# Kernel tuning notes

Hardware: AMD Instinct MI355X
Metric: run time of the kernel (lower is better)

Reference implementation:

```python
import jax, jax.numpy as jnp
import numpy as np

SCALE_CLS = 7.0
EPS = 1e-12

def _l2norm(x):
    # torch F.normalize: x / max(||x||_2, eps) along last dim
    n = jnp.sqrt(jnp.sum(x * x, axis=-1, keepdims=True))
    return x / jnp.maximum(n, EPS)

def setup_inputs() -> dict:
    key = jax.random.key(0)
    k1, k2 = jax.random.split(key)
    B, Q, C, D, H, W = 4, 75, 5, 512, 6, 6
    ftrain = jax.random.normal(k1, (B, Q, C, D, H, W), dtype=jnp.float32)
    ftest = jax.random.normal(k2, (B, Q, C, D, H, W), dtype=jnp.float32)
    return {"ftrain": ftrain, "ftest": ftest, "K": 28}

def reference(ftrain, ftest, K):
    B, Q, C, D, H, W = ftrain.shape
    P = H * W  # 36 spatial positions
    # spatial means -> [B,Q,C,1,D]
    ftest_mean = ftest.mean(axis=(4, 5))[:, :, :, None, :]
    ftrain_mean = ftrain.mean(axis=(4, 5))[:, :, :, None, :]
    # flatten spatial, move channel last -> [B,Q,C,P,D]
    ft = jnp.swapaxes(ftest.reshape(B, Q, C, D, P), 3, 4)
    fr = jnp.swapaxes(ftrain.reshape(B, Q, C, D, P), 3, 4)
    ft = _l2norm(ft)
    fr = _l2norm(fr)
    ftest_mean = _l2norm(ftest_mean)
    ftrain_mean = _l2norm(ftrain_mean)
    # global scores [B,Q,C]
    scores = SCALE_CLS * jnp.sum(jnp.squeeze(ftest_mean * ftrain_mean), axis=-1)
    # per-position scores [B,Q,C,P]
    ftrain_scores = SCALE_CLS * jnp.sum(ftest_mean * fr, axis=-1)
    ftest_scores = SCALE_CLS * jnp.sum(ft * ftrain_mean, axis=-1)
    # top-K positions (indices distinct, so one-hot-sum mask == gather)
    _, train_ind = jax.lax.top_k(ftrain_scores, K)  # [B,Q,C,K]
    _, test_ind = jax.lax.top_k(ftest_scores, K)
    # gather top-K spatial features and average -> [B,Q,C,D]
    ftest_fuse = jnp.take_along_axis(ft, test_ind[..., None], axis=3).sum(axis=3) / K
    ftrain_fuse = jnp.take_along_axis(fr, train_ind[..., None], axis=3).sum(axis=3) / K
    ftest_fuse = _l2norm(ftest_fuse)
    ftrain_fuse = _l2norm(ftrain_fuse)
    scores_final = SCALE_CLS * jnp.sum(ftest_fuse * ftrain_fuse, axis=-1)
    return (scores, scores_final)
```

## Files before the change

kernel.cpp:

```cpp
#include <hip/hip_runtime.h>
#include <stdint.h>

#define NGRP 1500
#define DD   512
#define PP   36
#define DP   (DD*PP)
#define NT   512
#define SCALE_CLS 7.0f
#define EPS 1e-12f

__device__ __forceinline__ float waveRed(float x){
  #pragma unroll
  for (int off = 32; off; off >>= 1) x += __shfl_xor(x, off, 64);
  return x;
}

__global__ __launch_bounds__(NT, 4)
void topk_fuse(const float* __restrict__ gtrain,
               const float* __restrict__ gtest,
               const int* __restrict__ Kp,
               float* __restrict__ out)
{
  __shared__ float sR[DP];
  __shared__ float s_tm[DD];
  __shared__ float s_q4[4][PP];
  __shared__ float s_a4[4][PP];
  __shared__ float s_e[PP], s_b[PP];
  __shared__ float s_nt[PP], s_nr[PP];
  __shared__ float s_st[PP], s_sr[PP];
  __shared__ __align__(16) float s_wt[PP];
  __shared__ __align__(16) float s_wr[PP];
  __shared__ float s_red[24];

  const int t    = threadIdx.x;
  const int lane = t & 63;
  const int wave = t >> 6;
  const int g    = blockIdx.x;
  const int K    = Kp[0];

  float4 rowT[9];
  {
    const float4* gTrow = (const float4*)(gtest + (size_t)g * DP + (size_t)t * PP);
    #pragma unroll
    for (int i = 0; i < 9; ++i) rowT[i] = gTrow[i];
  }
  {
    const float4* gR4 = (const float4*)(gtrain + (size_t)g * DP);
    float4 r0=gR4[t],        r1=gR4[t+NT],   r2=gR4[t+2*NT], r3=gR4[t+3*NT],
           r4=gR4[t+4*NT],   r5=gR4[t+5*NT], r6=gR4[t+6*NT], r7=gR4[t+7*NT],
           r8=gR4[t+8*NT];
    float4* sR4 = (float4*)sR;
    sR4[t]      = r0; sR4[t+NT]   = r1; sR4[t+2*NT] = r2; sR4[t+3*NT] = r3;
    sR4[t+4*NT] = r4; sR4[t+5*NT] = r5; sR4[t+6*NT] = r6; sR4[t+7*NT] = r7;
    sR4[t+8*NT] = r8;
  }

  if (t < PP) {
    s_e[t] = 0.f; s_b[t] = 0.f;
    #pragma unroll
    for (int v = 0; v < 4; ++v) { s_q4[v][t] = 0.f; s_a4[v][t] = 0.f; }
  }

  float acc = 0.f;
  #pragma unroll
  for (int i = 0; i < 9; ++i) { float4 x = rowT[i]; acc += (x.x + x.y) + (x.z + x.w); }
  const float tm = acc * (1.0f / 36.0f);
  s_tm[t] = tm;

  __syncthreads();

  const float4* rr4 = (const float4*)(sR + t * PP);
  float accr = 0.f;
  #pragma unroll
  for (int i = 0; i < 9; ++i) { float4 y = rr4[i]; accr += (y.x + y.y) + (y.z + y.w); }
  const float rm = accr * (1.0f / 36.0f);

  {
    float pm2 = waveRed(tm * tm);
    float pr2 = waveRed(rm * rm);
    float pmr = waveRed(tm * rm);
    if (lane == 0) { s_red[wave] = pm2; s_red[8+wave] = pr2; s_red[16+wave] = pmr; }
  }

  {
    const int slot = (lane >> 2) & 3;
    #pragma unroll
    for (int i = 0; i < 9; ++i) {
      float4 x = rowT[i];
      #pragma unroll
      for (int cpt = 0; cpt < 4; ++cpt) {
        const float xv = (cpt == 0) ? x.x : (cpt == 1) ? x.y : (cpt == 2) ? x.z : x.w;
        const int p = 4 * i + cpt;
        float q = xv * xv;
        float a = xv * rm;
        q += __shfl_xor(q, 1, 64); q += __shfl_xor(q, 2, 64);
        a += __shfl_xor(a, 1, 64); a += __shfl_xor(a, 2, 64);
        if ((lane & 3) == 0) {
          atomicAdd(&s_q4[slot][p], q);
          atomicAdd(&s_a4[slot][p], a);
        }
      }
    }
  }

  if (t < 504) {
    const int p = t % 36, c = t / 36;
    float e = 0.f, bb = 0.f;
    for (int d = c; d < DD; d += 14) {
      float y = sR[d * PP + p];
      e  += y * y;
      bb += y * s_tm[d];
    }
    atomicAdd(&s_e[p], e); atomicAdd(&s_b[p], bb);
  }
  __syncthreads();

  if (t == 0) {
    float m2 = 0.f, r2 = 0.f, mr = 0.f;
    #pragma unroll
    for (int w = 0; w < 8; ++w) { m2 += s_red[w]; r2 += s_red[8+w]; mr += s_red[16+w]; }
    out[g] = SCALE_CLS * mr / (fmaxf(sqrtf(m2), EPS) * fmaxf(sqrtf(r2), EPS));
  }

  if (wave < 2 && lane < PP) {
    float q, dm;
    if (wave) { q = s_e[lane]; dm = s_b[lane]; }
    else {
      q  = s_q4[0][lane] + s_q4[1][lane] + s_q4[2][lane] + s_q4[3][lane];
      dm = s_a4[0][lane] + s_a4[1][lane] + s_a4[2][lane] + s_a4[3][lane];
    }
    float n  = fmaxf(sqrtf(q), EPS);
    float sc = dm / n;
    if (wave) { s_nr[lane] = n; s_sr[lane] = sc; }
    else      { s_nt[lane] = n; s_st[lane] = sc; }
  }
  __syncthreads();

  if (wave < 2 && lane < PP) {
    const float* sc = wave ? s_sr : s_st;
    const float* nn = wave ? s_nr : s_nt;
    float*       w  = wave ? s_wr : s_wt;
    float mine = sc[lane];
    int rank = 0;
    #pragma unroll
    for (int p = 0; p < PP; ++p) {
      float o = sc[p];
      rank += ((o > mine) || (o == mine && p < lane)) ? 1 : 0;
    }
    w[lane] = (rank < K) ? (1.0f / nn[lane]) : 0.f;
  }
  __syncthreads();

  {
    const float4* w4t = (const float4*)s_wt;
    const float4* w4r = (const float4*)s_wr;
    float U = 0.f, V = 0.f;
    #pragma unroll
    for (int i = 0; i < 9; ++i) {
      float4 x = rowT[i], wa = w4t[i];
      float4 y = rr4[i],  wb = w4r[i];
      U += x.x*wa.x + x.y*wa.y + x.z*wa.z + x.w*wa.w;
      V += y.x*wb.x + y.y*wb.y + y.z*wb.z + y.w*wb.w;
    }
    float u2 = waveRed(U * U);
    float v2 = waveRed(V * V);
    float uv = waveRed(U * V);
    if (lane == 0) { s_red[wave] = u2; s_red[8+wave] = v2; s_red[16+wave] = uv; }
  }
  __syncthreads();
  if (t == 0) {
    float u2 = 0.f, v2 = 0.f, uv = 0.f;
    #pragma unroll
    for (int w = 0; w < 8; ++w) { u2 += s_red[w]; v2 += s_red[8+w]; uv += s_red[16+w]; }
    out[NGRP + g] = SCALE_CLS * uv / (fmaxf(sqrtf(u2), EPS) * fmaxf(sqrtf(v2), EPS));
  }
}

extern "C" void kernel_launch(void* const* d_in, const int* in_sizes, int n_in,
                              void* d_out, int out_size, void* d_ws, size_t ws_size,
                              hipStream_t stream)
{
  const float* ftrain = (const float*)d_in[0];
  const float* ftest  = (const float*)d_in[1];
  const int*   Kp     = (const int*)d_in[2];
  float*       out    = (float*)d_out;
  topk_fuse<<<NGRP, NT, 0, stream>>>(ftrain, ftest, Kp, out);
}
```

Before: 299.4 us.

## Compute all scores from a 72x72 Gram matrix of stacked test/train features

Result: faster. 258.3 us (-13.7%).

```diff
diff --git a/kernel.cpp b/kernel.cpp
--- a/kernel.cpp
+++ b/kernel.cpp
@@ -4,8 +4,13 @@
 #define NGRP 1500
 #define DD   512
 #define PP   36
+#define MW   72
 #define DP   (DD*PP)
-#define NT   512
+#define KC   64
+#define NCH  (DD/KC)
+#define NT   192
+#define NTILE 171
+#define F4C  (KC*PP/4)
 #define SCALE_CLS 7.0f
 #define EPS 1e-12f
 
@@ -21,16 +26,15 @@
                const int* __restrict__ Kp,
                float* __restrict__ out)
 {
-  __shared__ float sR[DP];
-  __shared__ float s_tm[DD];
-  __shared__ float s_q4[4][PP];
-  __shared__ float s_a4[4][PP];
-  __shared__ float s_e[PP], s_b[PP];
+  __shared__ __align__(16) float sM[KC][MW];
+  __shared__ float s_q[PP], s_e[PP];
+  __shared__ float s_a[PP], s_b[PP];
   __shared__ float s_nt[PP], s_nr[PP];
   __shared__ float s_st[PP], s_sr[PP];
-  __shared__ __align__(16) float s_wt[PP];
-  __shared__ __align__(16) float s_wr[PP];
-  __shared__ float s_red[24];
+  __shared__ __align__(16) float s_x[MW];
+  __shared__ __align__(16) float s_y[MW];
+  __shared__ float s_sums[3];
+  __shared__ float s_uvw[3];
 
   const int t    = threadIdx.x;
   const int lane = t & 63;
@@ -38,97 +42,101 @@
   const int g    = blockIdx.x;
   const int K    = Kp[0];
 
-  float4 rowT[9];
-  {
-    const float4* gTrow = (const float4*)(gtest + (size_t)g * DP + (size_t)t * PP);
-    #pragma unroll
-    for (int i = 0; i < 9; ++i) rowT[i] = gTrow[i];
-  }
-  {
-    const float4* gR4 = (const float4*)(gtrain + (size_t)g * DP);
-    float4 r0=gR4[t],        r1=gR4[t+NT],   r2=gR4[t+2*NT], r3=gR4[t+3*NT],
-           r4=gR4[t+4*NT],   r5=gR4[t+5*NT], r6=gR4[t+6*NT], r7=gR4[t+7*NT],
-           r8=gR4[t+8*NT];
-    float4* sR4 = (float4*)sR;
-    sR4[t]      = r0; sR4[t+NT]   = r1; sR4[t+2*NT] = r2; sR4[t+3*NT] = r3;
-    sR4[t+4*NT] = r4; sR4[t+5*NT] = r5; sR4[t+6*NT] = r6; sR4[t+7*NT] = r7;
-    sR4[t+8*NT] = r8;
-  }
-
-  if (t < PP) {
-    s_e[t] = 0.f; s_b[t] = 0.f;
-    #pragma unroll
-    for (int v = 0; v < 4; ++v) { s_q4[v][t] = 0.f; s_a4[v][t] = 0.f; }
-  }
-
-  float acc = 0.f;
-  #pragma unroll
-  for (int i = 0; i < 9; ++i) { float4 x = rowT[i]; acc += (x.x + x.y) + (x.z + x.w); }
-  const float tm = acc * (1.0f / 36.0f);
-  s_tm[t] = tm;
-
-  __syncthreads();
-
-  const float4* rr4 = (const float4*)(sR + t * PP);
-  float accr = 0.f;
-  #pragma unroll
-  for (int i = 0; i < 9; ++i) { float4 y = rr4[i]; accr += (y.x + y.y) + (y.z + y.w); }
-  const float rm = accr * (1.0f / 36.0f);
-
-  {
-    float pm2 = waveRed(tm * tm);
-    float pr2 = waveRed(rm * rm);
-    float pmr = waveRed(tm * rm);
-    if (lane == 0) { s_red[wave] = pm2; s_red[8+wave] = pr2; s_red[16+wave] = pmr; }
-  }
-
-  {
-    const int slot = (lane >> 2) & 3;
-    #pragma unroll
-    for (int i = 0; i < 9; ++i) {
-      float4 x = rowT[i];
+  int I = 0;
+  { int rem = (t < NTILE) ? t : 0;
+    if (t < NTILE) { while (rem >= 18 - I) { rem -= 18 - I; ++I; } }
+    else rem = 0;
+    (void)rem;
+  }
+  int J;
+  { int rem = t; int ii = 0;
+    if (t < NTILE) { while (rem >= 18 - ii) { rem -= 18 - ii; ++ii; } J = ii + rem; I = ii; }
+    else { I = 0; J = 0; }
+  }
+
+  if (t < PP) { s_a[t] = 0.f; s_b[t] = 0.f; }
+  if (t < 3)  { s_sums[t] = 0.f; s_uvw[t] = 0.f; }
+
+  const float4* gT4 = (const float4*)(gtest  + (size_t)g * DP);
+  const float4* gR4 = (const float4*)(gtrain + (size_t)g * DP);
+
+  float* wT0 = &sM[(t        )/9][((t        )%9)*4];
+  float* wT1 = &sM[(t +   NT )/9][((t +   NT )%9)*4];
+  float* wT2 = &sM[(t + 2*NT )/9][((t + 2*NT )%9)*4];
+
+  float acc[4][4] = {{0.f}};
+
+  float4 vT0 = gT4[t], vT1 = gT4[t+NT], vT2 = gT4[t+2*NT];
+  float4 vR0 = gR4[t], vR1 = gR4[t+NT], vR2 = gR4[t+2*NT];
+
+  for (int c = 0; c < NCH; ++c) {
+    *(float4*)(wT0)      = vT0; *(float4*)(wT1)      = vT1; *(float4*)(wT2)      = vT2;
+    *(float4*)(wT0 + 36) = vR0; *(float4*)(wT1 + 36) = vR1; *(float4*)(wT2 + 36) = vR2;
+
+    if (c + 1 < NCH) {
+      const int nb = (c + 1) * F4C;
+      vT0 = gT4[nb+t]; vT1 = gT4[nb+t+NT]; vT2 = gT4[nb+t+2*NT];
+      vR0 = gR4[nb+t]; vR1 = gR4[nb+t+NT]; vR2 = gR4[nb+t+2*NT];
+    }
+    __syncthreads();
+
+    if (t < NTILE) {
+      const float* mI = &sM[0][4*I];
+      const float* mJ = &sM[0][4*J];
+      #pragma unroll 4
+      for (int k = 0; k < KC; ++k) {
+        const float4 u = *(const float4*)(mI + k*MW);
+        const float4 v = *(const float4*)(mJ + k*MW);
+        acc[0][0] += u.x*v.x; acc[0][1] += u.x*v.y; acc[0][2] += u.x*v.z; acc[0][3] += u.x*v.w;
+        acc[1][0] += u.y*v.x; acc[1][1] += u.y*v.y; acc[1][2] += u.y*v.z; acc[1][3] += u.y*v.w;
+        acc[2][0] += u.z*v.x; acc[2][1] += u.z*v.y; acc[2][2] += u.z*v.z; acc[2][3] += u.z*v.w;
+        acc[3][0] += u.w*v.x; acc[3][1] += u.w*v.y; acc[3][2] += u.w*v.z; acc[3][3] += u.w*v.w;
+      }
+    }
+    __syncthreads();
+  }
+
+  if (t < NTILE) {
+    float rs0 = acc[0][0]+acc[0][1]+acc[0][2]+acc[0][3];
+    float rs1 = acc[1][0]+acc[1][1]+acc[1][2]+acc[1][3];
+    float rs2 = acc[2][0]+acc[2][1]+acc[2][2]+acc[2][3];
+    float rs3 = acc[3][0]+acc[3][1]+acc[3][2]+acc[3][3];
+    float tsum = rs0 + rs1 + rs2 + rs3;
+    if (J < 9) {
+      atomicAdd(&s_sums[0], (I == J) ? tsum : 2.f * tsum);
+    } else if (I >= 9) {
+      atomicAdd(&s_sums[2], (I == J) ? tsum : 2.f * tsum);
+    } else {
+      atomicAdd(&s_sums[1], tsum);
+      atomicAdd(&s_a[4*I+0], rs0); atomicAdd(&s_a[4*I+1], rs1);
+      atomicAdd(&s_a[4*I+2], rs2); atomicAdd(&s_a[4*I+3], rs3);
       #pragma unroll
-      for (int cpt = 0; cpt < 4; ++cpt) {
-        const float xv = (cpt == 0) ? x.x : (cpt == 1) ? x.y : (cpt == 2) ? x.z : x.w;
-        const int p = 4 * i + cpt;
-        float q = xv * xv;
-        float a = xv * rm;
-        q += __shfl_xor(q, 1, 64); q += __shfl_xor(q, 2, 64);
-        a += __shfl_xor(a, 1, 64); a += __shfl_xor(a, 2, 64);
-        if ((lane & 3) == 0) {
-          atomicAdd(&s_q4[slot][p], q);
-          atomicAdd(&s_a4[slot][p], a);
-        }
+      for (int cc = 0; cc < 4; ++cc) {
+        float cs = acc[0][cc]+acc[1][cc]+acc[2][cc]+acc[3][cc];
+        atomicAdd(&s_b[4*(J-9)+cc], cs);
       }
     }
-  }
-
-  if (t < 504) {
-    const int p = t % 36, c = t / 36;
-    float e = 0.f, bb = 0.f;
-    for (int d = c; d < DD; d += 14) {
-      float y = sR[d * PP + p];
-      e  += y * y;
-      bb += y * s_tm[d];
-    }
-    atomicAdd(&s_e[p], e); atomicAdd(&s_b[p], bb);
+    if (I == J) {
+      if (I < 9) {
+        s_q[4*I+0]=acc[0][0]; s_q[4*I+1]=acc[1][1]; s_q[4*I+2]=acc[2][2]; s_q[4*I+3]=acc[3][3];
+      } else {
+        s_e[4*(I-9)+0]=acc[0][0]; s_e[4*(I-9)+1]=acc[1][1];
+        s_e[4*(I-9)+2]=acc[2][2]; s_e[4*(I-9)+3]=acc[3][3];
+      }
+    }
   }
   __syncthreads();
 
   if (t == 0) {
-    float m2 = 0.f, r2 = 0.f, mr = 0.f;
-    #pragma unroll
-    for (int w = 0; w < 8; ++w) { m2 += s_red[w]; r2 += s_red[8+w]; mr += s_red[16+w]; }
+    float m2 = s_sums[0] * (1.f/1296.f);
+    float r2 = s_sums[2] * (1.f/1296.f);
+    float mr = s_sums[1] * (1.f/1296.f);
     out[g] = SCALE_CLS * mr / (fmaxf(sqrtf(m2), EPS) * fmaxf(sqrtf(r2), EPS));
   }
 
   if (wave < 2 && lane < PP) {
-    float q, dm;
-    if (wave) { q = s_e[lane]; dm = s_b[lane]; }
-    else {
-      q  = s_q4[0][lane] + s_q4[1][lane] + s_q4[2][lane] + s_q4[3][lane];
-      dm = s_a4[0][lane] + s_a4[1][lane] + s_a4[2][lane] + s_a4[3][lane];
-    }
+    float q  = wave ? s_e[lane] : s_q[lane];
+    float dm = wave ? s_b[lane] : s_a[lane];
     float n  = fmaxf(sqrtf(q), EPS);
     float sc = dm / n;
     if (wave) { s_nr[lane] = n; s_sr[lane] = sc; }
@@ -139,7 +147,6 @@
   if (wave < 2 && lane < PP) {
     const float* sc = wave ? s_sr : s_st;
     const float* nn = wave ? s_nr : s_nt;
-    float*       w  = wave ? s_wr : s_wt;
     float mine = sc[lane];
     int rank = 0;
     #pragma unroll
@@ -147,32 +154,57 @@
       float o = sc[p];
       rank += ((o > mine) || (o == mine && p < lane)) ? 1 : 0;
     }
-    w[lane] = (rank < K) ? (1.0f / nn[lane]) : 0.f;
-  }
-  __syncthreads();
-
-  {
-    const float4* w4t = (const float4*)s_wt;
-    const float4* w4r = (const float4*)s_wr;
-    float U = 0.f, V = 0.f;
+    float w = (rank < K) ? (1.0f / nn[lane]) : 0.f;
+    if (wave) s_y[36 + lane] = w;
+    else      s_x[lane]      = w;
+  }
+  if (wave == 2 && lane < PP) { s_x[36 + lane] = 0.f; s_y[lane] = 0.f; }
+  __syncthreads();
+
+  float u2 = 0.f, v2 = 0.f, uvv = 0.f;
+  if (t < NTILE) {
+    float xi[4], xj[4], yi[4], yj[4];
     #pragma unroll
-    for (int i = 0; i < 9; ++i) {
-      float4 x = rowT[i], wa = w4t[i];
-      float4 y = rr4[i],  wb = w4r[i];
-      U += x.x*wa.x + x.y*wa.y + x.z*wa.z + x.w*wa.w;
-      V += y.x*wb.x + y.y*wb.y + y.z*wb.z + y.w*wb.w;
-    }
-    float u2 = waveRed(U * U);
-    float v2 = waveRed(V * V);
-    float uv = waveRed(U * V);
-    if (lane == 0) { s_red[wave] = u2; s_red[8+wave] = v2; s_red[16+wave] = uv; }
-  }
-  __syncthreads();
+    for (int r = 0; r < 4; ++r) {
+      xi[r] = s_x[4*I+r]; xj[r] = s_x[4*J+r];
+      yi[r] = s_y[4*I+r]; yj[r] = s_y[4*J+r];
+    }
+    if (I == J) {
+      #pragma unroll
+      for (int r = 0; r < 4; ++r)
+        #pragma unroll
+        for (int cc = 0; cc < 4; ++cc) {
+          float A = acc[r][cc];
+          u2  += xi[r] * A * xi[cc];
+          v2  += yi[r] * A * yi[cc];
+          uvv += xi[r] * A * yi[cc];
+        }
+    } else {
+      #pragma unroll
+      for (int r = 0; r < 4; ++r)
+        #pragma unroll
+        for (int cc = 0; cc < 4; ++cc) {
+          float A = acc[r][cc];
+          u2  += 2.f * xi[r] * A * xj[cc];
+          v2  += 2.f * yi[r] * A * yj[cc];
+          uvv += xi[r] * A * yj[cc] + yi[r] * A * xj[cc];
+        }
+    }
+  }
+  u2  = waveRed(u2);
+  v2  = waveRed(v2);
+  uvv = waveRed(uvv);
+  if (lane == 0) {
+    atomicAdd(&s_uvw[0], u2);
+    atomicAdd(&s_uvw[1], v2);
+    atomicAdd(&s_uvw[2], uvv);
+  }
+  __syncthreads();
+
   if (t == 0) {
-    float u2 = 0.f, v2 = 0.f, uv = 0.f;
-    #pragma unroll
-    for (int w = 0; w < 8; ++w) { u2 += s_red[w]; v2 += s_red[8+w]; uv += s_red[16+w]; }
-    out[NGRP + g] = SCALE_CLS * uv / (fmaxf(sqrtf(u2), EPS) * fmaxf(sqrtf(v2), EPS));
+    float nu = fmaxf(sqrtf(s_uvw[0]), EPS);
+    float nv = fmaxf(sqrtf(s_uvw[1]), EPS);
+    out[NGRP + g] = SCALE_CLS * s_uvw[2] / (nu * nv);
   }
 }
 
```
